# Kernel tuning notes

Hardware: AMD Instinct MI355X
Metric: run time of the kernel (lower is better)

Reference implementation:

```python
import jax, jax.numpy as jnp
import numpy as np

B = 256          # batch of images
TOK = 256        # 16x16 tokens per image
V = 1024         # codebook size
D = 256          # code dim


def setup_inputs() -> dict:
    key = jax.random.key(0)
    k1, k2, k3, k4 = jax.random.split(key, 4)
    image_seq = jax.random.randint(k1, (B, TOK), 0, V, dtype=jnp.int64)
    image_seq2 = jax.random.randint(k2, (B, TOK), 0, V, dtype=jnp.int64)
    alpha = jax.random.uniform(k3, (1,), dtype=jnp.float32)
    W = jax.random.normal(k4, (V, D), dtype=jnp.float32)
    return {"image_seq": image_seq, "image_seq2": image_seq2, "alpha": alpha, "W": W}


def reference(image_seq, image_seq2, alpha, W):
    a = alpha[0]
    # gather codebook entries: [B, TOK, D]
    emb = W[image_seq]
    emb2 = W[image_seq2]
    x = (1.0 - a) * emb + a * emb2
    xf = x.reshape(-1, D)                        # [N, D], N = B*TOK
    # brute-force L2 distance to every code, without materializing [N, V, D]:
    d = (jnp.sum(xf * xf, axis=-1, keepdims=True)
         - 2.0 * xf @ W.T
         + jnp.sum(W * W, axis=-1)[None, :])
    idx = jnp.argmin(d, axis=1)                  # top-1 nearest code, [N]
    # get_codebook_entry: gather, reshape to bhwc, permute to bchw
    z_q = W[idx].reshape(B, 16, 16, D)           # [B, 16, 16, 256]
    z_q = jnp.transpose(z_q, (0, 3, 1, 2))       # [B, 256, 16, 16]
    return z_q
```

## Files before the change

kernel.cpp:

```cpp
#include <hip/hip_runtime.h>

static constexpr int Vn = 1024;
static constexpr int Dn = 256;
static constexpr int NT = 65536;

__global__ __launch_bounds__(256) void gram_kernel(const float* __restrict__ W,
                                                   float* __restrict__ G) {
    __shared__ float As[16][65];
    __shared__ float Bs[16][65];
    const int tid = threadIdx.x;
    const int tx = tid & 15;
    const int ty = tid >> 4;
    const int bm = blockIdx.y * 64;
    const int bn = blockIdx.x * 64;
    float acc[4][4] = {};
    for (int k0 = 0; k0 < Dn; k0 += 16) {
#pragma unroll
        for (int s = 0; s < 4; ++s) {
            int e = tid + 256 * s;
            int m = e >> 4;
            int k = e & 15;
            As[k][m] = W[(bm + m) * Dn + k0 + k];
            Bs[k][m] = W[(bn + m) * Dn + k0 + k];
        }
        __syncthreads();
#pragma unroll
        for (int kk = 0; kk < 16; ++kk) {
            float a[4], b[4];
#pragma unroll
            for (int u = 0; u < 4; ++u) a[u] = As[kk][ty * 4 + u];
#pragma unroll
            for (int u = 0; u < 4; ++u) b[u] = Bs[kk][tx * 4 + u];
#pragma unroll
            for (int u = 0; u < 4; ++u)
#pragma unroll
                for (int w = 0; w < 4; ++w)
                    acc[u][w] = fmaf(a[u], b[w], acc[u][w]);
        }
        __syncthreads();
    }
#pragma unroll
    for (int u = 0; u < 4; ++u) {
        const int row = bm + ty * 4 + u;
#pragma unroll
        for (int w = 0; w < 4; ++w) {
            G[row * Vn + bn + tx * 4 + w] = acc[u][w];
        }
    }
}

__global__ void diag_kernel(const float* __restrict__ G, float* __restrict__ norms) {
    const int v = blockIdx.x * 256 + threadIdx.x;
    norms[v] = G[v * (Vn + 1)];
}

__global__ __launch_bounds__(256) void argmin_kernel(const int* __restrict__ seq,
                                                     const int* __restrict__ seq2,
                                                     const float* __restrict__ alpha,
                                                     const float* __restrict__ G,
                                                     const float* __restrict__ norms,
                                                     int* __restrict__ out_idx) {
    __shared__ float nrm[Vn];
    const int tid = threadIdx.x;
    {
        const float4* n4 = (const float4*)norms;
        float4* s4 = (float4*)nrm;
        s4[tid] = n4[tid];
    }
    __syncthreads();
    const float a = alpha[0];
    const float c0 = -2.0f * (1.0f - a);
    const float c1 = -2.0f * a;
    const int wave = tid >> 6;
    const int lane = tid & 63;
    const int base_t = blockIdx.x * 16 + wave * 4;
    const float4* nr = (const float4*)nrm;
    for (int q = 0; q < 4; ++q) {
        const int t = base_t + q;
        const int i = seq[t];
        const int j = seq2[t];
        const float4* Gi = (const float4*)(G + i * Vn);
        const float4* Gj = (const float4*)(G + j * Vn);
        float best = __builtin_inff();
        int bestV = 0;
#pragma unroll
        for (int s = 0; s < 4; ++s) {
            const int e = s * 64 + lane;
            const float4 gi = Gi[e];
            const float4 gj = Gj[e];
            const float4 nn = nr[e];
            const float sc0 = fmaf(c1, gj.x, fmaf(c0, gi.x, nn.x));
            const float sc1 = fmaf(c1, gj.y, fmaf(c0, gi.y, nn.y));
            const float sc2 = fmaf(c1, gj.z, fmaf(c0, gi.z, nn.z));
            const float sc3 = fmaf(c1, gj.w, fmaf(c0, gi.w, nn.w));
            const int v = e * 4;
            if (sc0 < best) { best = sc0; bestV = v; }
            if (sc1 < best) { best = sc1; bestV = v + 1; }
            if (sc2 < best) { best = sc2; bestV = v + 2; }
            if (sc3 < best) { best = sc3; bestV = v + 3; }
        }
#pragma unroll
        for (int off = 32; off >= 1; off >>= 1) {
            const float ob = __shfl_down(best, off, 64);
            const int   ov = __shfl_down(bestV, off, 64);
            if (ob < best || (ob == best && ov < bestV)) { best = ob; bestV = ov; }
        }
        if (lane == 0) out_idx[t] = bestV;
    }
}

__global__ __launch_bounds__(256) void gather_transpose_kernel(const float* __restrict__ W,
                                                               const int* __restrict__ idx,
                                                               float* __restrict__ out) {
    __shared__ float tile[32][33];
    const int b   = blockIdx.z;
    const int hw0 = blockIdx.x * 32;
    const int d0  = blockIdx.y * 32;
    const int tx  = threadIdx.x & 31;
    const int ty  = threadIdx.x >> 5;
#pragma unroll
    for (int r = ty; r < 32; r += 8) {
        const int row = idx[b * 256 + hw0 + r];
        tile[r][tx] = W[row * Dn + d0 + tx];
    }
    __syncthreads();
#pragma unroll
    for (int r = ty; r < 32; r += 8) {
        out[b * 65536 + (d0 + r) * 256 + hw0 + tx] = tile[tx][r];
    }
}

extern "C" void kernel_launch(void* const* d_in, const int* in_sizes, int n_in,
                              void* d_out, int out_size, void* d_ws, size_t ws_size,
                              hipStream_t stream) {
    const int*   seq   = (const int*)d_in[0];
    const int*   seq2  = (const int*)d_in[1];
    const float* alpha = (const float*)d_in[2];
    const float* W     = (const float*)d_in[3];
    float* out = (float*)d_out;

    char* ws = (char*)d_ws;
    float* G     = (float*)ws;
    float* norms = (float*)(ws + (size_t)Vn * Vn * 4);
    int*   idx   = (int*)(ws + (size_t)Vn * Vn * 4 + Vn * 4);

    gram_kernel<<<dim3(16, 16), 256, 0, stream>>>(W, G);
    diag_kernel<<<Vn / 256, 256, 0, stream>>>(G, norms);
    argmin_kernel<<<NT / 16, 256, 0, stream>>>(seq, seq2, alpha, G, norms, idx);
    gather_transpose_kernel<<<dim3(8, 8, 256), 256, 0, stream>>>(W, idx, out);
}
```

Before: 145.7 us.

## Fuse diag into gram, retile gram and transpose, batch argmin row loads

```diff
diff --git a/kernel.cpp b/kernel.cpp
--- a/kernel.cpp
+++ b/kernel.cpp
@@ -5,53 +5,51 @@
 static constexpr int NT = 65536;
 
 __global__ __launch_bounds__(256) void gram_kernel(const float* __restrict__ W,
-                                                   float* __restrict__ G) {
-    __shared__ float As[16][65];
-    __shared__ float Bs[16][65];
+                                                   float* __restrict__ G,
+                                                   float* __restrict__ norms) {
+    __shared__ float As[32][33];
+    __shared__ float Bs[32][33];
     const int tid = threadIdx.x;
     const int tx = tid & 15;
     const int ty = tid >> 4;
-    const int bm = blockIdx.y * 64;
-    const int bn = blockIdx.x * 64;
-    float acc[4][4] = {};
-    for (int k0 = 0; k0 < Dn; k0 += 16) {
+    const int bm = blockIdx.y * 32;
+    const int bn = blockIdx.x * 32;
+    float acc[2][2] = {};
+    for (int k0 = 0; k0 < Dn; k0 += 32) {
 #pragma unroll
         for (int s = 0; s < 4; ++s) {
-            int e = tid + 256 * s;
-            int m = e >> 4;
-            int k = e & 15;
+            const int e = tid + 256 * s;
+            const int m = e >> 5;
+            const int k = e & 31;
             As[k][m] = W[(bm + m) * Dn + k0 + k];
             Bs[k][m] = W[(bn + m) * Dn + k0 + k];
         }
         __syncthreads();
 #pragma unroll
-        for (int kk = 0; kk < 16; ++kk) {
-            float a[4], b[4];
+        for (int kk = 0; kk < 32; ++kk) {
+            float a[2], b[2];
 #pragma unroll
-            for (int u = 0; u < 4; ++u) a[u] = As[kk][ty * 4 + u];
+            for (int u = 0; u < 2; ++u) a[u] = As[kk][ty + 16 * u];
 #pragma unroll
-            for (int u = 0; u < 4; ++u) b[u] = Bs[kk][tx * 4 + u];
+            for (int w = 0; w < 2; ++w) b[w] = Bs[kk][tx + 16 * w];
 #pragma unroll
-            for (int u = 0; u < 4; ++u)
+            for (int u = 0; u < 2; ++u)
 #pragma unroll
-                for (int w = 0; w < 4; ++w)
+                for (int w = 0; w < 2; ++w)
                     acc[u][w] = fmaf(a[u], b[w], acc[u][w]);
         }
         __syncthreads();
     }
 #pragma unroll
-    for (int u = 0; u < 4; ++u) {
-        const int row = bm + ty * 4 + u;
+    for (int u = 0; u < 2; ++u) {
+        const int row = bm + ty + 16 * u;
 #pragma unroll
-        for (int w = 0; w < 4; ++w) {
-            G[row * Vn + bn + tx * 4 + w] = acc[u][w];
+        for (int w = 0; w < 2; ++w) {
+            const int col = bn + tx + 16 * w;
+            G[row * Vn + col] = acc[u][w];
+            if (row == col) norms[row] = acc[u][w];
         }
     }
-}
-
-__global__ void diag_kernel(const float* __restrict__ G, float* __restrict__ norms) {
-    const int v = blockIdx.x * 256 + threadIdx.x;
-    norms[v] = G[v * (Vn + 1)];
 }
 
 __global__ __launch_bounds__(256) void argmin_kernel(const int* __restrict__ seq,
@@ -63,9 +61,7 @@
     __shared__ float nrm[Vn];
     const int tid = threadIdx.x;
     {
-        const float4* n4 = (const float4*)norms;
-        float4* s4 = (float4*)nrm;
-        s4[tid] = n4[tid];
+        ((float4*)nrm)[tid] = ((const float4*)norms)[tid];
     }
     __syncthreads();
     const float a = alpha[0];
@@ -75,57 +71,86 @@
     const int lane = tid & 63;
     const int base_t = blockIdx.x * 16 + wave * 4;
     const float4* nr = (const float4*)nrm;
-    for (int q = 0; q < 4; ++q) {
-        const int t = base_t + q;
-        const int i = seq[t];
-        const int j = seq2[t];
-        const float4* Gi = (const float4*)(G + i * Vn);
-        const float4* Gj = (const float4*)(G + j * Vn);
-        float best = __builtin_inff();
-        int bestV = 0;
+    int iv[4], jv[4];
+#pragma unroll
+    for (int q = 0; q < 4; ++q) { iv[q] = seq[base_t + q]; jv[q] = seq2[base_t + q]; }
+#pragma unroll
+    for (int pair = 0; pair < 2; ++pair) {
+        const int qa = pair * 2, qb = pair * 2 + 1;
+        const float4* GiA = (const float4*)(G + iv[qa] * Vn);
+        const float4* GjA = (const float4*)(G + jv[qa] * Vn);
+        const float4* GiB = (const float4*)(G + iv[qb] * Vn);
+        const float4* GjB = (const float4*)(G + jv[qb] * Vn);
+        float4 gia[4], gja[4], gib[4], gjb[4];
 #pragma unroll
         for (int s = 0; s < 4; ++s) {
             const int e = s * 64 + lane;
-            const float4 gi = Gi[e];
-            const float4 gj = Gj[e];
+            gia[s] = GiA[e];
+            gja[s] = GjA[e];
+            gib[s] = GiB[e];
+            gjb[s] = GjB[e];
+        }
+        float bestA = __builtin_inff(), bestB = __builtin_inff();
+        int vA = 0, vB = 0;
+#pragma unroll
+        for (int s = 0; s < 4; ++s) {
+            const int e = s * 64 + lane;
             const float4 nn = nr[e];
-            const float sc0 = fmaf(c1, gj.x, fmaf(c0, gi.x, nn.x));
-            const float sc1 = fmaf(c1, gj.y, fmaf(c0, gi.y, nn.y));
-            const float sc2 = fmaf(c1, gj.z, fmaf(c0, gi.z, nn.z));
-            const float sc3 = fmaf(c1, gj.w, fmaf(c0, gi.w, nn.w));
             const int v = e * 4;
-            if (sc0 < best) { best = sc0; bestV = v; }
-            if (sc1 < best) { best = sc1; bestV = v + 1; }
-            if (sc2 < best) { best = sc2; bestV = v + 2; }
-            if (sc3 < best) { best = sc3; bestV = v + 3; }
+            {
+                const float s0 = fmaf(c1, gja[s].x, fmaf(c0, gia[s].x, nn.x));
+                const float s1 = fmaf(c1, gja[s].y, fmaf(c0, gia[s].y, nn.y));
+                const float s2 = fmaf(c1, gja[s].z, fmaf(c0, gia[s].z, nn.z));
+                const float s3 = fmaf(c1, gja[s].w, fmaf(c0, gia[s].w, nn.w));
+                if (s0 < bestA) { bestA = s0; vA = v; }
+                if (s1 < bestA) { bestA = s1; vA = v + 1; }
+                if (s2 < bestA) { bestA = s2; vA = v + 2; }
+                if (s3 < bestA) { bestA = s3; vA = v + 3; }
+            }
+            {
+                const float s0 = fmaf(c1, gjb[s].x, fmaf(c0, gib[s].x, nn.x));
+                const float s1 = fmaf(c1, gjb[s].y, fmaf(c0, gib[s].y, nn.y));
+                const float s2 = fmaf(c1, gjb[s].z, fmaf(c0, gib[s].z, nn.z));
+                const float s3 = fmaf(c1, gjb[s].w, fmaf(c0, gib[s].w, nn.w));
+                if (s0 < bestB) { bestB = s0; vB = v; }
+                if (s1 < bestB) { bestB = s1; vB = v + 1; }
+                if (s2 < bestB) { bestB = s2; vB = v + 2; }
+                if (s3 < bestB) { bestB = s3; vB = v + 3; }
+            }
         }
 #pragma unroll
         for (int off = 32; off >= 1; off >>= 1) {
-            const float ob = __shfl_down(best, off, 64);
-            const int   ov = __shfl_down(bestV, off, 64);
-            if (ob < best || (ob == best && ov < bestV)) { best = ob; bestV = ov; }
+            const float oa = __shfl_down(bestA, off, 64);
+            const int   va = __shfl_down(vA, off, 64);
+            if (oa < bestA || (oa == bestA && va < vA)) { bestA = oa; vA = va; }
+            const float ob = __shfl_down(bestB, off, 64);
+            const int   vb = __shfl_down(vB, off, 64);
+            if (ob < bestB || (ob == bestB && vb < vB)) { bestB = ob; vB = vb; }
         }
-        if (lane == 0) out_idx[t] = bestV;
+        if (lane == 0) {
+            out_idx[base_t + qa] = vA;
+            out_idx[base_t + qb] = vB;
+        }
     }
 }
 
 __global__ __launch_bounds__(256) void gather_transpose_kernel(const float* __restrict__ W,
                                                                const int* __restrict__ idx,
                                                                float* __restrict__ out) {
-    __shared__ float tile[32][33];
+    __shared__ float tile[64][65];
     const int b   = blockIdx.z;
-    const int hw0 = blockIdx.x * 32;
-    const int d0  = blockIdx.y * 32;
-    const int tx  = threadIdx.x & 31;
-    const int ty  = threadIdx.x >> 5;
+    const int hw0 = blockIdx.x * 64;
+    const int d0  = blockIdx.y * 64;
+    const int tx  = threadIdx.x & 63;
+    const int ty  = threadIdx.x >> 6;
 #pragma unroll
-    for (int r = ty; r < 32; r += 8) {
+    for (int r = ty; r < 64; r += 4) {
         const int row = idx[b * 256 + hw0 + r];
         tile[r][tx] = W[row * Dn + d0 + tx];
     }
     __syncthreads();
 #pragma unroll
-    for (int r = ty; r < 32; r += 8) {
+    for (int r = ty; r < 64; r += 4) {
         out[b * 65536 + (d0 + r) * 256 + hw0 + tx] = tile[tx][r];
     }
 }
@@ -140,12 +165,11 @@
     float* out = (float*)d_out;
 
     char* ws = (char*)d_ws;
-    float* G     = (float*)ws;
-    float* norms = (float*)(ws + (size_t)Vn * Vn * 4);
-    int*   idx   = (int*)(ws + (size_t)Vn * Vn * 4 + Vn * 4);
+    float* G     = (float*)(ws);
+    float* norms = (float*)(ws + 4194304);
+    int*   idx   = (int*)  (ws + 4198400);
 
-    gram_kernel<<<dim3(16, 16), 256, 0, stream>>>(W, G);
-    diag_kernel<<<Vn / 256, 256, 0, stream>>>(G, norms);
+    gram_kernel<<<dim3(32, 32), 256, 0, stream>>>(W, G, norms);
     argmin_kernel<<<NT / 16, 256, 0, stream>>>(seq, seq2, alpha, G, norms, idx);
-    gather_transpose_kernel<<<dim3(8, 8, 256), 256, 0, stream>>>(W, idx, out);
+    gather_transpose_kernel<<<dim3(4, 4, 256), 256, 0, stream>>>(W, idx, out);
 }
```

New measurement: 142.9 us. No clear change (-1.9%).
